# Kernel tuning notes

Measured on AMD Instinct MI355X. Metric: run time of the kernel, lower is better.

The kernel has to match this reference:

```python
import jax, jax.numpy as jnp
import numpy as np


def conv2d_same(x, w, b):
    # x: [B, Cin, H, W], w: [Cout, Cin, 3, 3]
    y = jax.lax.conv_general_dilated(
        x, w, window_strides=(1, 1), padding='SAME',
        dimension_numbers=('NCHW', 'OIHW', 'NCHW'))
    return y + b[None, :, None, None]


def setup_inputs() -> dict:
    key = jax.random.key(0)
    k0, k1, k2 = jax.random.split(key, 3)
    T, B, C_in, H, W = 8, 4, 64, 128, 128
    hid = 64
    xinp = jax.random.normal(k0, (T, B, C_in, H, W), dtype=jnp.float32)
    # seq: 3x3 conv C_in -> hid
    W_seq = jax.random.normal(k1, (hid, C_in, 3, 3), dtype=jnp.float32) * (1.0 / np.sqrt(C_in * 9))
    b_seq = jnp.zeros((hid,), dtype=jnp.float32)
    # ConvLSTM cell: 3x3 conv on concat(input, h) -> 4*hid gate channels (i, f, g, o)
    W_cell = jax.random.normal(k2, (4 * hid, 2 * hid, 3, 3), dtype=jnp.float32) * (1.0 / np.sqrt(2 * hid * 9))
    b_cell = jnp.zeros((4 * hid,), dtype=jnp.float32)
    return {'xinp': xinp, 'W_seq': W_seq, 'b_seq': b_seq, 'W_cell': W_cell, 'b_cell': b_cell}


def reference(xinp, W_seq, b_seq, W_cell, b_cell):
    T, B, C_in, H, W = xinp.shape
    hid = W_seq.shape[0]
    h0 = jnp.zeros((B, hid, H, W), dtype=xinp.dtype)
    c0 = jnp.zeros((B, hid, H, W), dtype=xinp.dtype)

    def step(carry, x_t):
        h, c = carry
        input_t = conv2d_same(x_t, W_seq, b_seq)               # seq(xinp[t])
        gates = conv2d_same(jnp.concatenate([input_t, h], axis=1), W_cell, b_cell)
        i, f, g, o = jnp.split(gates, 4, axis=1)
        c_new = jax.nn.sigmoid(f) * c + jax.nn.sigmoid(i) * jnp.tanh(g)
        h_new = jax.nn.sigmoid(o) * jnp.tanh(c_new)
        return (h_new, c_new), input_t

    (h_final, c_final), xout = jax.lax.scan(step, (h0, c0), xinp)
    return h_final, xout
```

## Files before the change

### kernel.cpp

```cpp
#include <hip/hip_runtime.h>
#include <math.h>

#define HWDIM 128
#define IMG   (HWDIM * HWDIM)
#define PLANE (4 * 64 * IMG)

typedef __attribute__((ext_vector_type(8))) short bf16x8;
typedef __attribute__((ext_vector_type(4))) float f32x4;
typedef __attribute__((ext_vector_type(4))) int   i32x4;

__device__ __forceinline__ unsigned short f2bf(float f) {
    unsigned u = __builtin_bit_cast(unsigned, f);
    u += 0x7FFFu + ((u >> 16) & 1u);
    return (unsigned short)(u >> 16);
}
__device__ __forceinline__ float bf2f(unsigned short h) {
    unsigned u = ((unsigned)h) << 16;
    return __builtin_bit_cast(float, u);
}
__device__ __forceinline__ float sigmoidf_(float x) {
    return 1.f / (1.f + __expf(-x));
}
__device__ __forceinline__ float tanhf_(float x) {
    return 1.f - 2.f / (__expf(2.f * x) + 1.f);
}

__global__ void prep_weights_kernel(const float* __restrict__ Wc,
                                    const float* __restrict__ Ws,
                                    unsigned short* __restrict__ Wg2,
                                    unsigned short* __restrict__ Ws2) {
    int i = blockIdx.x * 256 + threadIdx.x;
    if (i < 9 * 256 * 128) {
        int tap = i >> 15, r = i & 32767, co = r >> 7, ci = r & 127;
        Wg2[i] = f2bf(Wc[(co * 128 + ci) * 9 + tap]);
    }
    if (i < 9 * 64 * 64) {
        int tap = i / 4096, r = i & 4095, co = r >> 6, ci = r & 63;
        Ws2[i] = f2bf(Ws[(co * 64 + ci) * 9 + tap]);
    }
}

__global__ __launch_bounds__(512, 4) void seq_conv_all(
    const float* __restrict__ xinp,
    const unsigned short* __restrict__ Ws2,
    const float* __restrict__ bseq,
    float* __restrict__ xout)
{
    __shared__ __align__(16) unsigned short tile[4 * 130 * 76];

    const int tid = threadIdx.x;
    const int sub = blockIdx.x;
    const int bid = (sub & 7) * 256 + (sub >> 3);
    const int t  = bid >> 8;
    const int b  = (bid >> 6) & 3;
    const int yp = bid & 63;
    const int y0 = yp * 2;

    const float* xb = xinp + (size_t)t * PLANE + (size_t)b * 64 * IMG;

    float4 ga[8], gb[8];
    #pragma unroll
    for (int it = 0; it < 8; ++it) {
        int i = tid + it * 512;
        int xq = i & 31, cip = (i >> 5) & 31, ry = i >> 10;
        int gy = y0 - 1 + ry;
        int ci = cip * 2;
        float4 va = {0.f, 0.f, 0.f, 0.f}, vb = {0.f, 0.f, 0.f, 0.f};
        if ((unsigned)gy < 128u) {
            va = *(const float4*)(xb + (size_t)ci * IMG + gy * HWDIM + xq * 4);
            vb = *(const float4*)(xb + (size_t)(ci + 1) * IMG + gy * HWDIM + xq * 4);
        }
        ga[it] = va; gb[it] = vb;
    }
    #pragma unroll
    for (int it = 0; it < 8; ++it) {
        int i = tid + it * 512;
        int xq = i & 31, cip = (i >> 5) & 31, ry = i >> 10;
        int ci = cip * 2;
        const float* pa = (const float*)&ga[it];
        const float* pb = (const float*)&gb[it];
        #pragma unroll
        for (int j = 0; j < 4; ++j) {
            unsigned pk = (unsigned)f2bf(pa[j]) | ((unsigned)f2bf(pb[j]) << 16);
            *(unsigned*)(tile + (ry * 130 + 1 + xq * 4 + j) * 76 + ci) = pk;
        }
    }
    if (tid < 256) {
        int e = tid & 1, cip = (tid >> 1) & 31, ry = tid >> 6;
        int xt = e ? 129 : 0;
        *(unsigned*)(tile + (ry * 130 + xt) * 76 + cip * 2) = 0u;
    }
    __syncthreads();

    const int lane = tid & 63;
    const int wv = tid >> 6;
    const int w  = wv & 3;
    const int rh = wv >> 2;
    const int ln = lane & 15, lg = lane >> 4;

    f32x4 acc[8];
    #pragma unroll
    for (int n = 0; n < 8; ++n) acc[n] = (f32x4){0.f, 0.f, 0.f, 0.f};

    const unsigned short* wbase = Ws2 + (size_t)(w * 16 + ln) * 64 + lg * 8;
    auto WL = [&](int step) -> bf16x8 {
        int tap = step >> 1, kk = step & 1;
        return *(const bf16x8*)(wbase + tap * 4096 + kk * 32);
    };
    auto MS = [&](bf16x8 wf, int step) {
        int tap = step >> 1, kk = step & 1;
        int dy = tap / 3, dxx = tap % 3;
        #pragma unroll
        for (int n = 0; n < 8; ++n) {
            bf16x8 imf = *(const bf16x8*)(tile + ((rh + dy) * 130 + n * 16 + ln + dxx) * 76 + kk * 32 + lg * 8);
            acc[n] = __builtin_amdgcn_mfma_f32_16x16x32_bf16(wf, imf, acc[n], 0, 0, 0);
        }
    };
    bf16x8 wA = WL(0), wB;
    #pragma unroll
    for (int st = 0; st < 18; st += 2) {
        wB = WL(st + 1);
        MS(wA, st);
        if (st + 2 < 18) wA = WL(st + 2);
        MS(wB, st + 1);
    }

    float* xout_t = xout + (size_t)t * PLANE;
    const int co = w * 16 + lg * 4;
    const int gy = y0 + rh;
    #pragma unroll
    for (int r = 0; r < 4; ++r) {
        const float bv = bseq[co + r];
        float* dst = xout_t + ((size_t)b * 64 + co + r) * IMG + (size_t)gy * HWDIM;
        #pragma unroll
        for (int n = 0; n < 8; ++n)
            dst[n * 16 + ln] = acc[n][r] + bv;
    }
}

__global__ __launch_bounds__(512, 4) void gates_lstm_mfma(
    const float* __restrict__ xo,
    const unsigned short* __restrict__ hin,
    const unsigned short* __restrict__ Wg2,
    const float* __restrict__ bcell,
    unsigned short* __restrict__ hout,
    unsigned short* __restrict__ cbuf,
    float* __restrict__ h32)
{
    __shared__ __align__(16) unsigned short wlds[2][64][36];
    __shared__ __align__(16) unsigned short btile[6][66][36];

    const int tid = threadIdx.x;
    const int sub = blockIdx.x;
    const int bid = (sub & 7) * 128 + (sub >> 3);
    const int b  = bid >> 8;
    const int yq = (bid >> 3) & 31;
    const int xh = (bid >> 2) & 1;
    const int cg = bid & 3;
    const int y0 = yq * 4;
    const int x0 = xh * 64;

    const int lane = tid & 63;
    const int wv = tid >> 6;
    const int rh = wv >> 1;
    const int nh = wv & 1;
    const int ln = lane & 15, lg = lane >> 4;

    const size_t pixb = (size_t)b * 128 * 128;
    const float* xb = xo + (size_t)b * 64 * IMG;

    const int lco = (tid >> 2) & 63;
    const int sl  = tid & 3;
    const int gco = (lco >> 4) * 64 + cg * 16 + (lco & 15);
    const unsigned short* wsrcb = Wg2 + (size_t)gco * 128 + sl * 8;

    i32x4 av;
    float4 xa[3], xc[3];
    float  ea, eb;
    i32x4 bv[4];

    auto LOADA = [&](int tap, int kk) {
        if (tid < 256)
            av = *(const i32x4*)(wsrcb + (size_t)tap * 32768 + kk * 32);
    };
    auto WRITEA = [&](int buf) {
        if (tid < 256)
            *(i32x4*)(&wlds[buf][lco][sl * 8]) = av;
    };
    auto LOADB = [&](int kk) {
        if (kk < 2) {
            #pragma unroll
            for (int it = 0; it < 3; ++it) {
                int i = tid + it * 512;
                int xq = i & 15, cip = (i >> 4) & 15, ry = i >> 8;
                int gy = y0 - 1 + ry;
                int ci = kk * 32 + cip * 2;
                float4 va = {0.f, 0.f, 0.f, 0.f}, vb = {0.f, 0.f, 0.f, 0.f};
                if ((unsigned)gy < 128u) {
                    va = *(const float4*)(xb + (size_t)ci * IMG + gy * HWDIM + x0 + xq * 4);
                    vb = *(const float4*)(xb + (size_t)(ci + 1) * IMG + gy * HWDIM + x0 + xq * 4);
                }
                xa[it] = va; xc[it] = vb;
            }
            ea = 0.f; eb = 0.f;
            {
                int e = tid & 1, cip = (tid >> 1) & 15, ry = tid >> 5;
                int gx = x0 - 1 + (e ? 65 : 0);
                int gy = y0 - 1 + ry;
                int ci = kk * 32 + cip * 2;
                if (tid < 192 && (unsigned)gy < 128u && (unsigned)gx < 128u) {
                    ea = xb[(size_t)ci * IMG + gy * HWDIM + gx];
                    eb = xb[(size_t)(ci + 1) * IMG + gy * HWDIM + gx];
                }
            }
        } else {
            const unsigned short* src = hin + pixb * 64 + (kk & 1) * 32;
            #pragma unroll
            for (int it = 0; it < 4; ++it) {
                int i = tid + it * 512;
                i32x4 v = {0, 0, 0, 0};
                if (i < 1584) {
                    int g4 = i & 3, rem = i >> 2;
                    int pxt = rem % 66, ry = rem / 66;
                    int gy = y0 - 1 + ry, gxx = x0 - 1 + pxt;
                    if ((unsigned)gy < 128u && (unsigned)gxx < 128u)
                        v = *(const i32x4*)(src + ((size_t)gy * 128 + gxx) * 64 + g4 * 8);
                }
                bv[it] = v;
            }
        }
    };
    auto WRITEB = [&](int kk) {
        if (kk < 2) {
            #pragma unroll
            for (int it = 0; it < 3; ++it) {
                int i = tid + it * 512;
                int xq = i & 15, cip = (i >> 4) & 15, ry = i >> 8;
                const float* pa = (const float*)&xa[it];
                const float* pb = (const float*)&xc[it];
                #pragma unroll
                for (int j = 0; j < 4; ++j) {
                    unsigned pk = (unsigned)f2bf(pa[j]) | ((unsigned)f2bf(pb[j]) << 16);
                    *(unsigned*)(&btile[ry][1 + xq * 4 + j][cip * 2]) = pk;
                }
            }
            if (tid < 192) {
                int e = tid & 1, cip = (tid >> 1) & 15, ry = tid >> 5;
                unsigned pk = (unsigned)f2bf(ea) | ((unsigned)f2bf(eb) << 16);
                *(unsigned*)(&btile[ry][e ? 65 : 0][cip * 2]) = pk;
            }
        } else {
            #pragma unroll
            for (int it = 0; it < 4; ++it) {
                int i = tid + it * 512;
                if (i < 1584) {
                    int g4 = i & 3, rem = i >> 2;
                    int pxt = rem % 66, ry = rem / 66;
                    *(i32x4*)(&btile[ry][pxt][g4 * 8]) = bv[it];
                }
            }
        }
    };

    LOADA(0, 0);
    LOADB(0);
    WRITEA(0);
    WRITEB(0);
    __syncthreads();

    f32x4 acc[4][2];
    #pragma unroll
    for (int g = 0; g < 4; ++g)
        #pragma unroll
        for (int n = 0; n < 2; ++n) acc[g][n] = (f32x4){0.f, 0.f, 0.f, 0.f};

    for (int kk = 0; kk < 4; ++kk) {
        for (int tap = 0; tap < 9; ++tap) {
            const int s = kk * 9 + tap;
            const int buf = s & 1;
            if (s < 35) {
                const int ntap = (tap == 8) ? 0 : tap + 1;
                const int nkk  = (tap == 8) ? kk + 1 : kk;
                LOADA(ntap, nkk);
            }
            if (tap == 8 && kk < 3) LOADB(kk + 1);

            const int dy = tap / 3, dxx = tap % 3;
            bf16x8 wf[4];
            #pragma unroll
            for (int g = 0; g < 4; ++g)
                wf[g] = *(const bf16x8*)(&wlds[buf][g * 16 + ln][lg * 8]);
            #pragma unroll
            for (int n = 0; n < 2; ++n) {
                bf16x8 af = *(const bf16x8*)(&btile[rh + dy][nh * 32 + n * 16 + ln + dxx][lg * 8]);
                #pragma unroll
                for (int g = 0; g < 4; ++g)
                    acc[g][n] = __builtin_amdgcn_mfma_f32_16x16x32_bf16(af, wf[g], acc[g][n], 0, 0, 0);
            }

            if (s < 35) WRITEA((s + 1) & 1);
            if (tap == 8 && kk < 3) {
                __syncthreads();
                WRITEB(kk + 1);
            }
            if (s < 35) __syncthreads();
        }
    }

    const int ch = cg * 16 + ln;
    const int gy = y0 + rh;
    const float bi = bcell[ch], bf_ = bcell[64 + ch];
    const float bg = bcell[128 + ch], bo = bcell[192 + ch];

    #pragma unroll
    for (int n = 0; n < 2; ++n) {
        #pragma unroll
        for (int r = 0; r < 4; ++r) {
            const int col = x0 + nh * 32 + n * 16 + lg * 4 + r;
            float gi = acc[0][n][r] + bi;
            float gf = acc[1][n][r] + bf_;
            float gg = acc[2][n][r] + bg;
            float go = acc[3][n][r] + bo;
            float si = sigmoidf_(gi);
            float sf = sigmoidf_(gf);
            float tg = tanhf_(gg);
            float so = sigmoidf_(go);
            const size_t pixbase = pixb + (size_t)gy * 128 + col;
            const size_t cidx = pixbase * 64 + ch;
            float cold = bf2f(cbuf[cidx]);
            float cn = sf * cold + si * tg;
            cbuf[cidx] = f2bf(cn);
            float hv = so * tanhf_(cn);
            hout[cidx] = f2bf(hv);
            if (h32) h32[((size_t)b * 64 + ch) * IMG + (size_t)gy * HWDIM + col] = hv;
        }
    }
}

extern "C" void kernel_launch(void* const* d_in, const int* in_sizes, int n_in,
                              void* d_out, int out_size, void* d_ws, size_t ws_size,
                              hipStream_t stream) {
    const float* xinp   = (const float*)d_in[0];
    const float* W_seq  = (const float*)d_in[1];
    const float* b_seq  = (const float*)d_in[2];
    const float* W_cell = (const float*)d_in[3];
    const float* b_cell = (const float*)d_in[4];

    float* out     = (float*)d_out;
    float* h_final = out;
    float* xout    = out + PLANE;

    unsigned short* cbuf = (unsigned short*)d_ws;
    unsigned short* hb0  = cbuf + PLANE;
    unsigned short* hb1  = hb0 + PLANE;
    unsigned short* Wg2  = hb1 + PLANE;
    unsigned short* Ws2  = Wg2 + 9 * 256 * 128;
    unsigned short* hbufs[2] = { hb0, hb1 };

    hipMemsetAsync(hb0,  0, (size_t)PLANE * sizeof(unsigned short), stream);
    hipMemsetAsync(cbuf, 0, (size_t)PLANE * sizeof(unsigned short), stream);

    prep_weights_kernel<<<1152, 256, 0, stream>>>(W_cell, W_seq, Wg2, Ws2);

    seq_conv_all<<<2048, 512, 0, stream>>>(xinp, Ws2, b_seq, xout);

    for (int t = 0; t < 8; ++t) {
        gates_lstm_mfma<<<1024, 512, 0, stream>>>(
            xout + (size_t)t * PLANE, hbufs[t & 1], Wg2, b_cell,
            hbufs[(t + 1) & 1], cbuf,
            (t == 7) ? h_final : (float*)nullptr);
    }
}
```

Baseline: 514.3 us.

## Stage all nine weight taps per K-half in LDS to cut barriers

Replaces the per-tap double-buffered weight staging, which needed a barrier for every tap, with a layout that loads all nine taps for a 64-channel K half into LDS at once. The main loop now has four nine-tap phases with only a few barriers between them. Launch bounds drop from 4 to 1 blocks per CU, and LDS use grows to about 83KB per block, which lowers occupancy and adds register pressure from the nine staged weight vectors.

```diff
diff --git a/kernel.cpp b/kernel.cpp
--- a/kernel.cpp
+++ b/kernel.cpp
@@ -138,7 +138,7 @@
     }
 }
 
-__global__ __launch_bounds__(512, 4) void gates_lstm_mfma(
+__global__ __launch_bounds__(512, 1) void gates_lstm_mfma(
     const float* __restrict__ xo,
     const unsigned short* __restrict__ hin,
     const unsigned short* __restrict__ Wg2,
@@ -147,7 +147,7 @@
     unsigned short* __restrict__ cbuf,
     float* __restrict__ h32)
 {
-    __shared__ __align__(16) unsigned short wlds[2][64][36];
+    __shared__ __align__(16) unsigned short wlds[9][64][72];
     __shared__ __align__(16) unsigned short btile[6][66][36];
 
     const int tid = threadIdx.x;
@@ -169,24 +169,27 @@
     const size_t pixb = (size_t)b * 128 * 128;
     const float* xb = xo + (size_t)b * 64 * IMG;
 
-    const int lco = (tid >> 2) & 63;
-    const int sl  = tid & 3;
-    const int gco = (lco >> 4) * 64 + cg * 16 + (lco & 15);
-    const unsigned short* wsrcb = Wg2 + (size_t)gco * 128 + sl * 8;
-
-    i32x4 av;
+    const int wsl  = tid & 7;
+    const int wlco = tid >> 3;
+    const int wgco = (wlco >> 4) * 64 + cg * 16 + (wlco & 15);
+    const unsigned short* wsrc = Wg2 + (size_t)wgco * 128 + wsl * 8;
+
+    i32x4 wreg[9];
+    auto LOADW = [&](int kh) {
+        #pragma unroll
+        for (int tp = 0; tp < 9; ++tp)
+            wreg[tp] = *(const i32x4*)(wsrc + (size_t)tp * 32768 + kh * 64);
+    };
+    auto WRITEW = [&]() {
+        #pragma unroll
+        for (int tp = 0; tp < 9; ++tp)
+            *(i32x4*)(&wlds[tp][wlco][wsl * 8]) = wreg[tp];
+    };
+
     float4 xa[3], xc[3];
     float  ea, eb;
     i32x4 bv[4];
 
-    auto LOADA = [&](int tap, int kk) {
-        if (tid < 256)
-            av = *(const i32x4*)(wsrcb + (size_t)tap * 32768 + kk * 32);
-    };
-    auto WRITEA = [&](int buf) {
-        if (tid < 256)
-            *(i32x4*)(&wlds[buf][lco][sl * 8]) = av;
-    };
     auto LOADB = [&](int kk) {
         if (kk < 2) {
             #pragma unroll
@@ -262,9 +265,9 @@
         }
     };
 
-    LOADA(0, 0);
+    LOADW(0);
     LOADB(0);
-    WRITEA(0);
+    WRITEW();
     WRITEB(0);
     __syncthreads();
 
@@ -274,22 +277,14 @@
         #pragma unroll
         for (int n = 0; n < 2; ++n) acc[g][n] = (f32x4){0.f, 0.f, 0.f, 0.f};
 
-    for (int kk = 0; kk < 4; ++kk) {
+    auto NINETAPS = [&](int k2) {
+        #pragma unroll
         for (int tap = 0; tap < 9; ++tap) {
-            const int s = kk * 9 + tap;
-            const int buf = s & 1;
-            if (s < 35) {
-                const int ntap = (tap == 8) ? 0 : tap + 1;
-                const int nkk  = (tap == 8) ? kk + 1 : kk;
-                LOADA(ntap, nkk);
-            }
-            if (tap == 8 && kk < 3) LOADB(kk + 1);
-
             const int dy = tap / 3, dxx = tap % 3;
             bf16x8 wf[4];
             #pragma unroll
             for (int g = 0; g < 4; ++g)
-                wf[g] = *(const bf16x8*)(&wlds[buf][g * 16 + ln][lg * 8]);
+                wf[g] = *(const bf16x8*)(&wlds[tap][g * 16 + ln][k2 * 32 + lg * 8]);
             #pragma unroll
             for (int n = 0; n < 2; ++n) {
                 bf16x8 af = *(const bf16x8*)(&btile[rh + dy][nh * 32 + n * 16 + ln + dxx][lg * 8]);
@@ -297,15 +292,30 @@
                 for (int g = 0; g < 4; ++g)
                     acc[g][n] = __builtin_amdgcn_mfma_f32_16x16x32_bf16(af, wf[g], acc[g][n], 0, 0, 0);
             }
-
-            if (s < 35) WRITEA((s + 1) & 1);
-            if (tap == 8 && kk < 3) {
-                __syncthreads();
-                WRITEB(kk + 1);
-            }
-            if (s < 35) __syncthreads();
-        }
-    }
+        }
+    };
+
+    LOADB(1);
+    NINETAPS(0);
+    __syncthreads();
+    WRITEB(1);
+    __syncthreads();
+
+    LOADW(1);
+    LOADB(2);
+    NINETAPS(1);
+    __syncthreads();
+    WRITEW();
+    WRITEB(2);
+    __syncthreads();
+
+    LOADB(3);
+    NINETAPS(0);
+    __syncthreads();
+    WRITEB(3);
+    __syncthreads();
+
+    NINETAPS(1);
 
     const int ch = cg * 16 + ln;
     const int gy = y0 + rh;
```

New measurement: 787.1 us. +53.0%, slower.
